# Optimization experiments

Hardware: AMD Instinct MI355X
Metric: run time of the kernel (lower is better)

## Reference

```python
import jax, jax.numpy as jnp
import numpy as np
from jax import lax
from jax.scipy.special import logsumexp

NUM_STATES = 32
INPUT_SIZE = 128
HIDDEN = 256
LN_EPS = 1e-5


def setup_inputs() -> dict:
    key = jax.random.key(0)
    ks = jax.random.split(key, 8)
    B, T = 32, 8192
    x = jax.random.normal(ks[0], (B, T, INPUT_SIZE), dtype=jnp.float32)
    # parameters (match torch defaults: initial_logits=zeros, transition_logits=2*I)
    initial_logits = jnp.zeros((NUM_STATES,), jnp.float32)
    transition_logits = 2.0 * jnp.eye(NUM_STATES, dtype=jnp.float32)
    W1 = jax.random.normal(ks[1], (INPUT_SIZE, HIDDEN), jnp.float32) / np.sqrt(INPUT_SIZE)
    b1 = jnp.zeros((HIDDEN,), jnp.float32)
    ln_g = jnp.ones((HIDDEN,), jnp.float32)
    ln_b = jnp.zeros((HIDDEN,), jnp.float32)
    W2 = jax.random.normal(ks[2], (HIDDEN, HIDDEN), jnp.float32) / np.sqrt(HIDDEN)
    b2 = jnp.zeros((HIDDEN,), jnp.float32)
    W3 = jax.random.normal(ks[3], (HIDDEN, NUM_STATES), jnp.float32) / np.sqrt(HIDDEN)
    b3 = jnp.zeros((NUM_STATES,), jnp.float32)
    return {"x": x, "initial_logits": initial_logits, "transition_logits": transition_logits,
            "W1": W1, "b1": b1, "ln_g": ln_g, "ln_b": ln_b, "W2": W2, "b2": b2, "W3": W3, "b3": b3}


def _emission_logprobs(x, W1, b1, ln_g, ln_b, W2, b2, W3, b3):
    h = x @ W1 + b1                                   # (B,T,H)
    mu = h.mean(-1, keepdims=True)
    var = ((h - mu) ** 2).mean(-1, keepdims=True)
    h = (h - mu) * lax.rsqrt(var + LN_EPS) * ln_g + ln_b
    h = jax.nn.gelu(h, approximate=False)             # torch nn.GELU default = exact
    h = jax.nn.gelu(h @ W2 + b2, approximate=False)
    logits = h @ W3 + b3                              # (B,T,S)  (dropout inactive at eval)
    return jax.nn.log_softmax(logits, axis=-1)


def reference(x, initial_logits, transition_logits, W1, b1, ln_g, ln_b, W2, b2, W3, b3):
    emissions = _emission_logprobs(x, W1, b1, ln_g, ln_b, W2, b2, W3, b3)  # (B,T,S)
    B = x.shape[0]
    trans = jax.nn.softmax(transition_logits, axis=-1)
    log_trans = jnp.log(trans + 1e-10)                               # (S,S)
    log_init = jnp.log(jax.nn.softmax(initial_logits) + 1e-10)       # (S,)

    alpha0 = log_init[None, :] + emissions[:, 0, :]                  # (B,S)
    em_rest = jnp.swapaxes(emissions[:, 1:, :], 0, 1)                # (T-1,B,S)

    # --- forward algorithm (log-sum-exp semiring scan over time) ---
    def fwd_step(alpha, em_t):
        a = em_t + logsumexp(alpha[:, :, None] + log_trans[None, :, :], axis=1)
        return a, a
    _, alphas_rest = lax.scan(fwd_step, alpha0, em_rest)             # (T-1,B,S)
    alphas = jnp.concatenate([alpha0[:, None, :], jnp.swapaxes(alphas_rest, 0, 1)], axis=1)  # (B,T,S)
    log_likelihood = logsumexp(alphas[:, -1, :], axis=-1)            # (B,)
    state_probs = jax.nn.softmax(alphas, axis=-1)

    # --- Viterbi (max-plus semiring scan + backtrace) ---
    def vit_step(vit, em_t):
        scores = vit[:, :, None] + log_trans[None, :, :]             # (B,S,S)
        return scores.max(axis=1) + em_t, scores.argmax(axis=1)
    vit_last, bps = lax.scan(vit_step, alpha0, em_rest)              # bps: (T-1,B,S) int32
    path_score = vit_last.max(axis=-1)
    last_state = vit_last.argmax(axis=-1)                            # (B,)
    bidx = jnp.arange(B)

    def bt_step(state, bp):
        prev = bp[bidx, state]
        return prev, prev
    _, path_prefix = lax.scan(bt_step, last_state, bps, reverse=True)  # (T-1,B)
    best_path = jnp.concatenate([jnp.swapaxes(path_prefix, 0, 1), last_state[:, None]], axis=1)  # (B,T)

    return (emissions, state_probs, log_likelihood, trans, best_path, path_score)
```

## Files before the change

### kernel.cpp

```cpp
#include <hip/hip_runtime.h>
#include <cstdint>
#include <cstddef>

#define TT 8192
#define SS 32

__device__ __forceinline__ float rsum32(float v){
    v += __shfl_xor(v,16); v += __shfl_xor(v,8); v += __shfl_xor(v,4);
    v += __shfl_xor(v,2);  v += __shfl_xor(v,1); return v;
}
__device__ __forceinline__ float rmax32(float v){
    v = fmaxf(v,__shfl_xor(v,16)); v = fmaxf(v,__shfl_xor(v,8)); v = fmaxf(v,__shfl_xor(v,4));
    v = fmaxf(v,__shfl_xor(v,2));  v = fmaxf(v,__shfl_xor(v,1)); return v;
}
__device__ __forceinline__ float rsum64(float v){
    v += __shfl_xor(v,32); v += __shfl_xor(v,16); v += __shfl_xor(v,8);
    v += __shfl_xor(v,4);  v += __shfl_xor(v,2);  v += __shfl_xor(v,1); return v;
}
__device__ __forceinline__ void lds_read32(const float* p, float* d){
    #pragma unroll
    for (int k=0;k<8;k++){
        float4 v = ((const float4*)p)[k];
        d[4*k+0]=v.x; d[4*k+1]=v.y; d[4*k+2]=v.z; d[4*k+3]=v.w;
    }
}
__device__ __forceinline__ float arr_sum32(const float* a){
    float s0=0.f,s1=0.f,s2=0.f,s3=0.f;
    #pragma unroll
    for (int k=0;k<32;k+=4){ s0+=a[k]; s1+=a[k+1]; s2+=a[k+2]; s3+=a[k+3]; }
    return (s0+s1)+(s2+s3);
}
__device__ __forceinline__ float arr_max32(const float* a){
    float s0=a[0],s1=a[1],s2=a[2],s3=a[3];
    #pragma unroll
    for (int k=4;k<32;k+=4){ s0=fmaxf(s0,a[k]); s1=fmaxf(s1,a[k+1]); s2=fmaxf(s2,a[k+2]); s3=fmaxf(s3,a[k+3]); }
    return fmaxf(fmaxf(s0,s1),fmaxf(s2,s3));
}
__device__ __forceinline__ float dot32(const float* a, const float* b){
    float s0=0.f,s1=0.f,s2=0.f,s3=0.f;
    #pragma unroll
    for (int k=0;k<32;k+=4){
        s0=fmaf(a[k],b[k],s0); s1=fmaf(a[k+1],b[k+1],s1);
        s2=fmaf(a[k+2],b[k+2],s2); s3=fmaf(a[k+3],b[k+3],s3);
    }
    return (s0+s1)+(s2+s3);
}
__device__ __forceinline__ float gelu_exact(float v){
    return 0.5f*v*(1.0f + erff(v*0.70710678118654752440f));
}

__global__ __launch_bounds__(1024) void hmm_prep(
    const float* __restrict__ il, const float* __restrict__ tl,
    float* __restrict__ trans, float* __restrict__ lt, float* __restrict__ li,
    float* __restrict__ LL, float* __restrict__ PS)
{
    const int tid = threadIdx.x;
    const int c = tid & 31;
    const float v = tl[tid];
    const float m = rmax32(v);
    const float e = expf(v - m);
    const float ssum = rsum32(e);
    const float t = e / ssum;
    trans[tid] = t;
    lt[tid] = logf(t + 1e-10f);
    if (tid < 32){
        const float iv = il[c];
        const float m2 = rmax32(iv);
        const float e2 = expf(iv - m2);
        const float s2 = rsum32(e2);
        li[c] = logf(e2/s2 + 1e-10f);
        LL[c] = 0.f;
        PS[c] = 0.f;
    }
}

__global__ __launch_bounds__(256, 5) void hmm_mlp(
    const float* __restrict__ x,
    const float* __restrict__ W1, const float* __restrict__ b1,
    const float* __restrict__ lng, const float* __restrict__ lnb,
    const float* __restrict__ W2, const float* __restrict__ b2,
    const float* __restrict__ W3, const float* __restrict__ b3,
    float* __restrict__ em_out)
{
    __shared__ float hbuf[8192];
    const int tid  = threadIdx.x;
    const int lane = tid & 63;
    const int wv   = tid >> 6;
    const int row0 = blockIdx.x << 5;
    const int r0   = wv << 3;
    const int c0   = lane << 2;

    const int r0u = __builtin_amdgcn_readfirstlane(r0);
    const float* xw = x + ((size_t)(row0 + r0u) << 7);

    float acc[8][4];
    #pragma unroll
    for (int i=0;i<8;i++){ acc[i][0]=0.f; acc[i][1]=0.f; acc[i][2]=0.f; acc[i][3]=0.f; }

    #pragma unroll 2
    for (int k4=0;k4<32;k4++){
        const float4 w0 = *(const float4*)&W1[((k4<<2)+0)*256 + c0];
        const float4 w1 = *(const float4*)&W1[((k4<<2)+1)*256 + c0];
        const float4 w2 = *(const float4*)&W1[((k4<<2)+2)*256 + c0];
        const float4 w3 = *(const float4*)&W1[((k4<<2)+3)*256 + c0];
        #pragma unroll
        for (int i=0;i<8;i++){
            const float4 xv = *(const float4*)(xw + (i<<7) + (k4<<2));
            acc[i][0]=fmaf(xv.x,w0.x,acc[i][0]); acc[i][1]=fmaf(xv.x,w0.y,acc[i][1]);
            acc[i][2]=fmaf(xv.x,w0.z,acc[i][2]); acc[i][3]=fmaf(xv.x,w0.w,acc[i][3]);
            acc[i][0]=fmaf(xv.y,w1.x,acc[i][0]); acc[i][1]=fmaf(xv.y,w1.y,acc[i][1]);
            acc[i][2]=fmaf(xv.y,w1.z,acc[i][2]); acc[i][3]=fmaf(xv.y,w1.w,acc[i][3]);
            acc[i][0]=fmaf(xv.z,w2.x,acc[i][0]); acc[i][1]=fmaf(xv.z,w2.y,acc[i][1]);
            acc[i][2]=fmaf(xv.z,w2.z,acc[i][2]); acc[i][3]=fmaf(xv.z,w2.w,acc[i][3]);
            acc[i][0]=fmaf(xv.w,w3.x,acc[i][0]); acc[i][1]=fmaf(xv.w,w3.y,acc[i][1]);
            acc[i][2]=fmaf(xv.w,w3.z,acc[i][2]); acc[i][3]=fmaf(xv.w,w3.w,acc[i][3]);
        }
    }

    {
        const float4 bb = *(const float4*)&b1[c0];
        const float4 gg = *(const float4*)&lng[c0];
        const float4 be = *(const float4*)&lnb[c0];
        #pragma unroll
        for (int i=0;i<8;i++){
            float a0=acc[i][0]+bb.x, a1=acc[i][1]+bb.y, a2=acc[i][2]+bb.z, a3=acc[i][3]+bb.w;
            float sm = (a0+a1)+(a2+a3);
            float sq = fmaf(a0,a0,fmaf(a1,a1,fmaf(a2,a2,a3*a3)));
            sm = rsum64(sm); sq = rsum64(sq);
            const float mu   = sm*(1.f/256.f);
            const float var  = sq*(1.f/256.f) - mu*mu;
            const float rstd = rsqrtf(var + 1e-5f);
            a0 = gelu_exact((a0-mu)*rstd*gg.x + be.x);
            a1 = gelu_exact((a1-mu)*rstd*gg.y + be.y);
            a2 = gelu_exact((a2-mu)*rstd*gg.z + be.z);
            a3 = gelu_exact((a3-mu)*rstd*gg.w + be.w);
            *(float4*)&hbuf[(r0+i)*256 + c0] = make_float4(a0,a1,a2,a3);
        }
    }

    #pragma unroll
    for (int i=0;i<8;i++){ acc[i][0]=0.f; acc[i][1]=0.f; acc[i][2]=0.f; acc[i][3]=0.f; }
    #pragma unroll 2
    for (int k4=0;k4<64;k4++){
        const float4 w0 = *(const float4*)&W2[((k4<<2)+0)*256 + c0];
        const float4 w1 = *(const float4*)&W2[((k4<<2)+1)*256 + c0];
        const float4 w2 = *(const float4*)&W2[((k4<<2)+2)*256 + c0];
        const float4 w3 = *(const float4*)&W2[((k4<<2)+3)*256 + c0];
        #pragma unroll
        for (int i=0;i<8;i++){
            const float4 hv = *(const float4*)&hbuf[(r0+i)*256 + (k4<<2)];
            acc[i][0]=fmaf(hv.x,w0.x,acc[i][0]); acc[i][1]=fmaf(hv.x,w0.y,acc[i][1]);
            acc[i][2]=fmaf(hv.x,w0.z,acc[i][2]); acc[i][3]=fmaf(hv.x,w0.w,acc[i][3]);
            acc[i][0]=fmaf(hv.y,w1.x,acc[i][0]); acc[i][1]=fmaf(hv.y,w1.y,acc[i][1]);
            acc[i][2]=fmaf(hv.y,w1.z,acc[i][2]); acc[i][3]=fmaf(hv.y,w1.w,acc[i][3]);
            acc[i][0]=fmaf(hv.z,w2.x,acc[i][0]); acc[i][1]=fmaf(hv.z,w2.y,acc[i][1]);
            acc[i][2]=fmaf(hv.z,w2.z,acc[i][2]); acc[i][3]=fmaf(hv.z,w2.w,acc[i][3]);
            acc[i][0]=fmaf(hv.w,w3.x,acc[i][0]); acc[i][1]=fmaf(hv.w,w3.y,acc[i][1]);
            acc[i][2]=fmaf(hv.w,w3.z,acc[i][2]); acc[i][3]=fmaf(hv.w,w3.w,acc[i][3]);
        }
    }
    {
        const float4 bv = *(const float4*)&b2[c0];
        #pragma unroll
        for (int i=0;i<8;i++){
            const int r = r0+i;
            const float a0 = gelu_exact(acc[i][0]+bv.x);
            const float a1 = gelu_exact(acc[i][1]+bv.y);
            const float a2 = gelu_exact(acc[i][2]+bv.z);
            const float a3 = gelu_exact(acc[i][3]+bv.w);
            *(float4*)&hbuf[r*256 + (c0 ^ ((r&7)<<2))] = make_float4(a0,a1,a2,a3);
        }
    }

    {
        const int r3  = tid >> 3;
        const int cg  = tid & 7;
        const int sw3 = (r3 & 7) << 2;
        float a3[4] = {0.f,0.f,0.f,0.f};
        const float4* W34 = (const float4*)W3;
        #pragma unroll 2
        for (int k4=0;k4<64;k4++){
            const float4 hv = *(const float4*)&hbuf[r3*256 + ((k4<<2) ^ sw3)];
            const float h[4] = {hv.x,hv.y,hv.z,hv.w};
            #pragma unroll
            for (int kk=0;kk<4;kk++){
                const float4 w = W34[((k4<<2)+kk)*8 + cg];
                a3[0]=fmaf(h[kk],w.x,a3[0]); a3[1]=fmaf(h[kk],w.y,a3[1]);
                a3[2]=fmaf(h[kk],w.z,a3[2]); a3[3]=fmaf(h[kk],w.w,a3[3]);
            }
        }
        const float4 b3v = ((const float4*)b3)[cg];
        a3[0]+=b3v.x; a3[1]+=b3v.y; a3[2]+=b3v.z; a3[3]+=b3v.w;
        float m = fmaxf(fmaxf(a3[0],a3[1]),fmaxf(a3[2],a3[3]));
        m = fmaxf(m,__shfl_xor(m,4)); m = fmaxf(m,__shfl_xor(m,2)); m = fmaxf(m,__shfl_xor(m,1));
        float se = expf(a3[0]-m)+expf(a3[1]-m)+expf(a3[2]-m)+expf(a3[3]-m);
        se += __shfl_xor(se,4); se += __shfl_xor(se,2); se += __shfl_xor(se,1);
        const float lz = m + logf(se);
        float4 o = make_float4(a3[0]-lz, a3[1]-lz, a3[2]-lz, a3[3]-lz);
        *(float4*)&em_out[((size_t)(row0+r3))*32 + (cg<<2)] = o;
    }
}

__global__ __launch_bounds__(256) void hmm_fwd(
    const float* __restrict__ em, const float* __restrict__ trans,
    const float* __restrict__ li, float* __restrict__ sp, float* __restrict__ LL)
{
    __shared__ float Ab[8][32];
    const int lane = threadIdx.x & 63;
    const int s = lane & 31;
    const int ci = ((threadIdx.x >> 6) << 1) | (lane >> 5);
    const int cid = (blockIdx.x << 3) + ci;
    const int b = cid >> 7;
    const int c = cid & 127;
    const int t0 = c << 6;

    float tc[32];
    #pragma unroll
    for (int k=0;k<32;k++) tc[k] = trans[(k<<5) + s];
    float* A = Ab[ci];
    const float* emb = em + (size_t)b*(TT*SS);
    const float li_s = li[s];

    A[s] = 0.03125f;
    asm volatile("s_waitcnt lgkmcnt(0)" ::: "memory");
    __builtin_amdgcn_wave_barrier();

    float sig = 0.f;
    float araw_prev = 0.f;

    const int tws = t0 - 64;
    float pe[8];
    #pragma unroll
    for (int j=0;j<8;j++){ int tt = tws + j; tt = tt < 0 ? 0 : tt; pe[j] = emb[(tt<<5) + s]; }

    #pragma unroll 1
    for (int g=0; g<8; g++){
        float ce[8];
        #pragma unroll
        for (int j=0;j<8;j++) ce[j] = pe[j];
        #pragma unroll
        for (int j=0;j<8;j++){ int tt = tws + ((g+1)<<3) + j; tt = tt < 0 ? 0 : tt; pe[j] = emb[(tt<<5) + s]; }
        #pragma unroll
        for (int j=0;j<8;j++){
            float Av[32];
            lds_read32(A, Av);
            const float sum = arr_sum32(Av);
            const float val = dot32(Av, tc);
            const float rs = 1.0f / sum;
            const float e = __expf(ce[j]);
            const float araw = val * rs * e;
            __builtin_amdgcn_wave_barrier();
            A[s] = araw;
            asm volatile("s_waitcnt lgkmcnt(0)" ::: "memory");
            __builtin_amdgcn_wave_barrier();
        }
    }

    #pragma unroll 1
    for (int g=0; g<8; g++){
        float ce[8];
        #pragma unroll
        for (int j=0;j<8;j++) ce[j] = pe[j];
        #pragma unroll
        for (int j=0;j<8;j++){ int tt = t0 + ((g+1)<<3) + j; tt = tt > (TT-1) ? (TT-1) : tt; pe[j] = emb[(tt<<5) + s]; }
        #pragma unroll
        for (int j=0;j<8;j++){
            const int i = (g<<3) + j;
            const int t = t0 + i;
            float Av[32];
            lds_read32(A, Av);
            const float sum = arr_sum32(Av);
            const float val = dot32(Av, tc);
            const float rs = 1.0f / sum;
            if (i > 0){
                sp[((size_t)b*TT + (t-1))*SS + s] = araw_prev * rs;
                sig += __logf(sum);
            }
            const float e = __expf(ce[j]);
            float araw = val * rs * e;
            if (c == 0 && i == 0) araw = __expf(li_s) * e;
            __builtin_amdgcn_wave_barrier();
            A[s] = araw;
            asm volatile("s_waitcnt lgkmcnt(0)" ::: "memory");
            __builtin_amdgcn_wave_barrier();
            araw_prev = araw;
        }
    }
    {
        float Av[32];
        lds_read32(A, Av);
        const float sum = arr_sum32(Av);
        const float rs = 1.0f / sum;
        sp[((size_t)b*TT + (t0+63))*SS + s] = araw_prev * rs;
        sig += __logf(sum);
    }
    if (s == 0) atomicAdd(&LL[b], sig);
}

__global__ __launch_bounds__(256) void hmm_vit(
    const float* __restrict__ em, const float* __restrict__ lt,
    const float* __restrict__ li, unsigned char* __restrict__ bps,
    float* __restrict__ PS, int* __restrict__ last_state)
{
    __shared__ float Vb[8][32];
    const int lane = threadIdx.x & 63;
    const int s = lane & 31;
    const int ci = ((threadIdx.x >> 6) << 1) | (lane >> 5);
    const int cid = (blockIdx.x << 3) + ci;
    const int b = cid >> 7;
    const int c = cid & 127;
    const int t0 = c << 6;

    float ltc[32];
    #pragma unroll
    for (int k=0;k<32;k++) ltc[k] = lt[(k<<5) + s];
    float* V = Vb[ci];
    const float* emb = em + (size_t)b*(TT*SS);
    const float li_s = li[s];

    V[s] = 0.f;
    asm volatile("s_waitcnt lgkmcnt(0)" ::: "memory");
    __builtin_amdgcn_wave_barrier();

    float delta = 0.f;

    const int tws = t0 - 128;
    float pe[8];
    #pragma unroll
    for (int j=0;j<8;j++){ int tt = tws + j; tt = tt < 0 ? 0 : tt; pe[j] = emb[(tt<<5) + s]; }

    #pragma unroll 1
    for (int g=0; g<16; g++){
        float ce[8];
        #pragma unroll
        for (int j=0;j<8;j++) ce[j] = pe[j];
        #pragma unroll
        for (int j=0;j<8;j++){ int tt = tws + ((g+1)<<3) + j; tt = tt < 0 ? 0 : tt; pe[j] = emb[(tt<<5) + s]; }
        #pragma unroll
        for (int j=0;j<8;j++){
            float Vv[32];
            lds_read32(V, Vv);
            float b0=-3.0e38f,b1v=-3.0e38f,b2v=-3.0e38f,b3v=-3.0e38f;
            #pragma unroll
            for (int k=0;k<32;k+=4){
                b0  = fmaxf(b0,  Vv[k]+ltc[k]);
                b1v = fmaxf(b1v, Vv[k+1]+ltc[k+1]);
                b2v = fmaxf(b2v, Vv[k+2]+ltc[k+2]);
                b3v = fmaxf(b3v, Vv[k+3]+ltc[k+3]);
            }
            float v = fmaxf(fmaxf(b0,b1v),fmaxf(b2v,b3v)) + ce[j];
            if (j == 7) v -= arr_max32(Vv);
            __builtin_amdgcn_wave_barrier();
            V[s] = v;
            asm volatile("s_waitcnt lgkmcnt(0)" ::: "memory");
            __builtin_amdgcn_wave_barrier();
        }
    }
    {
        float Vv[32];
        lds_read32(V, Vv);
        const float mm = arr_max32(Vv);
        __builtin_amdgcn_wave_barrier();
        V[s] = Vv[s] - mm;
        asm volatile("s_waitcnt lgkmcnt(0)" ::: "memory");
        __builtin_amdgcn_wave_barrier();
    }

    #pragma unroll 1
    for (int g=0; g<8; g++){
        float ce[8];
        #pragma unroll
        for (int j=0;j<8;j++) ce[j] = pe[j];
        #pragma unroll
        for (int j=0;j<8;j++){ int tt = t0 + ((g+1)<<3) + j; tt = tt > (TT-1) ? (TT-1) : tt; pe[j] = emb[(tt<<5) + s]; }
        #pragma unroll
        for (int j=0;j<8;j++){
            const int i = (g<<3) + j;
            const int t = t0 + i;
            float Vv[32];
            lds_read32(V, Vv);
            float B0=Vv[0]+ltc[0], B1=Vv[1]+ltc[1], B2=Vv[2]+ltc[2], B3=Vv[3]+ltc[3];
            int I0=0,I1=1,I2=2,I3=3;
            #pragma unroll
            for (int k=4;k<32;k+=4){
                float q0=Vv[k]+ltc[k];     if (q0>B0){B0=q0;I0=k;}
                float q1=Vv[k+1]+ltc[k+1]; if (q1>B1){B1=q1;I1=k+1;}
                float q2=Vv[k+2]+ltc[k+2]; if (q2>B2){B2=q2;I2=k+2;}
                float q3=Vv[k+3]+ltc[k+3]; if (q3>B3){B3=q3;I3=k+3;}
            }
            float best = B0; int bi = I0;
            if (B1>best || (B1==best && I1<bi)){best=B1;bi=I1;}
            if (B2>best || (B2==best && I2<bi)){best=B2;bi=I2;}
            if (B3>best || (B3==best && I3<bi)){best=B3;bi=I3;}
            float mmc = 0.f;
            if (j == 0){ mmc = arr_max32(Vv); delta += mmc; }
            float v;
            if (c == 0 && i == 0){
                v = li_s + ce[j];
            } else {
                v = best + ce[j] - mmc;
                bps[((size_t)b*TT + t)*SS + s] = (unsigned char)bi;
            }
            __builtin_amdgcn_wave_barrier();
            V[s] = v;
            asm volatile("s_waitcnt lgkmcnt(0)" ::: "memory");
            __builtin_amdgcn_wave_barrier();
        }
    }
    {
        float Vv[32];
        lds_read32(V, Vv);
        const float mm = arr_max32(Vv);
        delta += mm;
        if (c == 127){
            float best = Vv[0]; int bi = 0;
            #pragma unroll
            for (int k=1;k<32;k++){ if (Vv[k] > best){ best = Vv[k]; bi = k; } }
            if (s == 0) last_state[b] = bi;
        }
        if (s == 0) atomicAdd(&PS[b], delta);
    }
}

__global__ __launch_bounds__(64) void hmm_btc(
    const unsigned char* __restrict__ bps, unsigned char* __restrict__ pos,
    unsigned char* __restrict__ gmap)
{
    __shared__ unsigned char bp[8192];
    const int b = blockIdx.x >> 5;
    const int cb = blockIdx.x & 31;
    const int tbase = cb << 8;
    {
        const uint4* src = (const uint4*)(bps + ((size_t)b*TT + tbase)*SS);
        uint4* dst = (uint4*)bp;
        #pragma unroll
        for (int l=0;l<8;l++) dst[threadIdx.x + (l<<6)] = src[threadIdx.x + (l<<6)];
    }
    __syncthreads();
    if (threadIdx.x < 32){
        int cur = threadIdx.x;
        unsigned char* pc = pos + (((size_t)b<<5) + cb)*8192;
        #pragma unroll 1
        for (int t=255; t>=0; t--){
            pc[(t<<5) + threadIdx.x] = (unsigned char)cur;
            if ((tbase + t) >= 1) cur = bp[(t<<5) + cur];
        }
        gmap[(((b<<5) + cb)<<5) + threadIdx.x] = (unsigned char)cur;
    }
}

__global__ __launch_bounds__(256) void hmm_btb(
    const unsigned char* __restrict__ gmap, const int* __restrict__ last_state,
    unsigned char* __restrict__ e_tab)
{
    __shared__ unsigned char gl[32768];
    #pragma unroll
    for (int l=0;l<8;l++) ((uint4*)gl)[threadIdx.x + (l<<8)] = ((const uint4*)gmap)[threadIdx.x + (l<<8)];
    __syncthreads();
    if (threadIdx.x < 32){
        const int b = threadIdx.x;
        int s = last_state[b];
        #pragma unroll 1
        for (int cb=31; cb>=1; cb--){
            e_tab[(b<<5)+cb] = (unsigned char)s;
            s = gl[(((b<<5)+cb)<<5) + s];
        }
        e_tab[b<<5] = (unsigned char)s;
    }
}

__global__ __launch_bounds__(256) void hmm_btf(
    const unsigned char* __restrict__ pos, const unsigned char* __restrict__ e_tab,
    float* __restrict__ path)
{
    const int i = blockIdx.x*256 + threadIdx.x;
    const int b = i >> 13;
    const int t = i & (TT-1);
    const int cb = t >> 8;
    const int e = e_tab[(b<<5) + cb];
    const unsigned char v = pos[((((size_t)b<<5) + cb)<<13) + ((t & 255)<<5) + e];
    path[i] = (float)v;
}

extern "C" void kernel_launch(void* const* d_in, const int* in_sizes, int n_in,
                              void* d_out, int out_size, void* d_ws, size_t ws_size,
                              hipStream_t stream)
{
    const float* x   = (const float*)d_in[0];
    const float* il  = (const float*)d_in[1];
    const float* tl  = (const float*)d_in[2];
    const float* W1  = (const float*)d_in[3];
    const float* b1  = (const float*)d_in[4];
    const float* lng = (const float*)d_in[5];
    const float* lnb = (const float*)d_in[6];
    const float* W2  = (const float*)d_in[7];
    const float* b2  = (const float*)d_in[8];
    const float* W3  = (const float*)d_in[9];
    const float* b3  = (const float*)d_in[10];

    float* out   = (float*)d_out;
    float* em    = out;
    float* sp    = out + 8388608;
    float* LL    = out + 16777216;
    float* trans = out + 16777248;
    float* path  = out + 16778272;
    float* PS    = out + 17040416;

    char* wsb = (char*)d_ws;
    float* lt            = (float*)(wsb);
    float* li            = (float*)(wsb + 4096);
    int* last_state      = (int*)(wsb + 4224);
    unsigned char* e_tab = (unsigned char*)(wsb + 4352);
    unsigned char* bps   = (unsigned char*)(wsb + 8192);
    unsigned char* pos   = (unsigned char*)(wsb + 8192 + 8388608);
    unsigned char* gmap  = (unsigned char*)(wsb + 8192 + 16777216);

    hmm_prep<<<1, 1024, 0, stream>>>(il, tl, trans, lt, li, LL, PS);
    hmm_mlp<<<8192, 256, 0, stream>>>(x, W1, b1, lng, lnb, W2, b2, W3, b3, em);
    hmm_fwd<<<512, 256, 0, stream>>>(em, trans, li, sp, LL);
    hmm_vit<<<512, 256, 0, stream>>>(em, lt, li, bps, PS, last_state);
    hmm_btc<<<1024, 64, 0, stream>>>(bps, pos, gmap);
    hmm_btb<<<1, 256, 0, stream>>>(gmap, last_state, e_tab);
    hmm_btf<<<1024, 256, 0, stream>>>(pos, e_tab, path);
}
```

Measured before the change: 1.432 ms.

## Give each MLP wave 16 rows with wave-private swizzled LDS and per-wave output layer

The MLP kernel drops from 256-thread blocks of four waves with 8 rows each to 128-thread blocks of two waves with 16 rows each. Each wave works on its own swizzled slice of LDS, so every W1/W2 weight load is reused across twice as many rows. The final 256x32 layer becomes a per-wave split-K over two half-warps combined with a shuffle, which removes the cross-wave LDS dependency. In exchange each thread holds 64 accumulators, which raises register pressure and lowers occupancy, and half the lanes sit idle during the output stores.

```diff
diff --git a/kernel.cpp b/kernel.cpp
--- a/kernel.cpp
+++ b/kernel.cpp
@@ -74,7 +74,7 @@
     }
 }
 
-__global__ __launch_bounds__(256, 5) void hmm_mlp(
+__global__ __launch_bounds__(128, 4) void hmm_mlp(
     const float* __restrict__ x,
     const float* __restrict__ W1, const float* __restrict__ b1,
     const float* __restrict__ lng, const float* __restrict__ lnb,
@@ -86,16 +86,15 @@
     const int tid  = threadIdx.x;
     const int lane = tid & 63;
     const int wv   = tid >> 6;
-    const int row0 = blockIdx.x << 5;
-    const int r0   = wv << 3;
-    const int c0   = lane << 2;
-
-    const int r0u = __builtin_amdgcn_readfirstlane(r0);
-    const float* xw = x + ((size_t)(row0 + r0u) << 7);
-
-    float acc[8][4];
-    #pragma unroll
-    for (int i=0;i<8;i++){ acc[i][0]=0.f; acc[i][1]=0.f; acc[i][2]=0.f; acc[i][3]=0.f; }
+    const int rowbase = (blockIdx.x << 5) + (wv << 4);
+    float* hb = hbuf + (wv << 12);
+    const int c0 = lane << 2;
+
+    const float* xw = x + ((size_t)__builtin_amdgcn_readfirstlane(rowbase) << 7);
+
+    float acc[16][4];
+    #pragma unroll
+    for (int i=0;i<16;i++){ acc[i][0]=0.f; acc[i][1]=0.f; acc[i][2]=0.f; acc[i][3]=0.f; }
 
     #pragma unroll 2
     for (int k4=0;k4<32;k4++){
@@ -104,7 +103,7 @@
         const float4 w2 = *(const float4*)&W1[((k4<<2)+2)*256 + c0];
         const float4 w3 = *(const float4*)&W1[((k4<<2)+3)*256 + c0];
         #pragma unroll
-        for (int i=0;i<8;i++){
+        for (int i=0;i<16;i++){
             const float4 xv = *(const float4*)(xw + (i<<7) + (k4<<2));
             acc[i][0]=fmaf(xv.x,w0.x,acc[i][0]); acc[i][1]=fmaf(xv.x,w0.y,acc[i][1]);
             acc[i][2]=fmaf(xv.x,w0.z,acc[i][2]); acc[i][3]=fmaf(xv.x,w0.w,acc[i][3]);
@@ -122,7 +121,7 @@
         const float4 gg = *(const float4*)&lng[c0];
         const float4 be = *(const float4*)&lnb[c0];
         #pragma unroll
-        for (int i=0;i<8;i++){
+        for (int i=0;i<16;i++){
             float a0=acc[i][0]+bb.x, a1=acc[i][1]+bb.y, a2=acc[i][2]+bb.z, a3=acc[i][3]+bb.w;
             float sm = (a0+a1)+(a2+a3);
             float sq = fmaf(a0,a0,fmaf(a1,a1,fmaf(a2,a2,a3*a3)));
@@ -134,12 +133,12 @@
             a1 = gelu_exact((a1-mu)*rstd*gg.y + be.y);
             a2 = gelu_exact((a2-mu)*rstd*gg.z + be.z);
             a3 = gelu_exact((a3-mu)*rstd*gg.w + be.w);
-            *(float4*)&hbuf[(r0+i)*256 + c0] = make_float4(a0,a1,a2,a3);
-        }
-    }
-
-    #pragma unroll
-    for (int i=0;i<8;i++){ acc[i][0]=0.f; acc[i][1]=0.f; acc[i][2]=0.f; acc[i][3]=0.f; }
+            *(float4*)&hb[(i<<8) + (c0 ^ ((i&7)<<2))] = make_float4(a0,a1,a2,a3);
+        }
+    }
+
+    #pragma unroll
+    for (int i=0;i<16;i++){ acc[i][0]=0.f; acc[i][1]=0.f; acc[i][2]=0.f; acc[i][3]=0.f; }
     #pragma unroll 2
     for (int k4=0;k4<64;k4++){
         const float4 w0 = *(const float4*)&W2[((k4<<2)+0)*256 + c0];
@@ -147,8 +146,8 @@
         const float4 w2 = *(const float4*)&W2[((k4<<2)+2)*256 + c0];
         const float4 w3 = *(const float4*)&W2[((k4<<2)+3)*256 + c0];
         #pragma unroll
-        for (int i=0;i<8;i++){
-            const float4 hv = *(const float4*)&hbuf[(r0+i)*256 + (k4<<2)];
+        for (int i=0;i<16;i++){
+            const float4 hv = *(const float4*)&hb[(i<<8) + (((k4<<2)) ^ ((i&7)<<2))];
             acc[i][0]=fmaf(hv.x,w0.x,acc[i][0]); acc[i][1]=fmaf(hv.x,w0.y,acc[i][1]);
             acc[i][2]=fmaf(hv.x,w0.z,acc[i][2]); acc[i][3]=fmaf(hv.x,w0.w,acc[i][3]);
             acc[i][0]=fmaf(hv.y,w1.x,acc[i][0]); acc[i][1]=fmaf(hv.y,w1.y,acc[i][1]);
@@ -162,42 +161,46 @@
     {
         const float4 bv = *(const float4*)&b2[c0];
         #pragma unroll
-        for (int i=0;i<8;i++){
-            const int r = r0+i;
+        for (int i=0;i<16;i++){
             const float a0 = gelu_exact(acc[i][0]+bv.x);
             const float a1 = gelu_exact(acc[i][1]+bv.y);
             const float a2 = gelu_exact(acc[i][2]+bv.z);
             const float a3 = gelu_exact(acc[i][3]+bv.w);
-            *(float4*)&hbuf[r*256 + (c0 ^ ((r&7)<<2))] = make_float4(a0,a1,a2,a3);
-        }
-    }
-
-    {
-        const int r3  = tid >> 3;
-        const int cg  = tid & 7;
-        const int sw3 = (r3 & 7) << 2;
-        float a3[4] = {0.f,0.f,0.f,0.f};
-        const float4* W34 = (const float4*)W3;
+            *(float4*)&hb[(i<<8) + (c0 ^ ((i&7)<<2))] = make_float4(a0,a1,a2,a3);
+        }
+    }
+
+    {
+        const int cS = lane & 31;
+        const int kh = lane >> 5;
+        float lg[16];
+        #pragma unroll
+        for (int i=0;i<16;i++) lg[i] = 0.f;
         #pragma unroll 2
-        for (int k4=0;k4<64;k4++){
-            const float4 hv = *(const float4*)&hbuf[r3*256 + ((k4<<2) ^ sw3)];
-            const float h[4] = {hv.x,hv.y,hv.z,hv.w};
+        for (int k4=0;k4<32;k4++){
+            const int kb = (kh<<7) + (k4<<2);
+            const int slot = (kb>>2);
+            const float wv0 = W3[(kb+0)*32 + cS];
+            const float wv1 = W3[(kb+1)*32 + cS];
+            const float wv2 = W3[(kb+2)*32 + cS];
+            const float wv3 = W3[(kb+3)*32 + cS];
             #pragma unroll
-            for (int kk=0;kk<4;kk++){
-                const float4 w = W34[((k4<<2)+kk)*8 + cg];
-                a3[0]=fmaf(h[kk],w.x,a3[0]); a3[1]=fmaf(h[kk],w.y,a3[1]);
-                a3[2]=fmaf(h[kk],w.z,a3[2]); a3[3]=fmaf(h[kk],w.w,a3[3]);
+            for (int i=0;i<16;i++){
+                const float4 hv = *(const float4*)&hb[(i<<8) + ((slot<<2) ^ ((i&7)<<2))];
+                lg[i]=fmaf(hv.x,wv0,lg[i]); lg[i]=fmaf(hv.y,wv1,lg[i]);
+                lg[i]=fmaf(hv.z,wv2,lg[i]); lg[i]=fmaf(hv.w,wv3,lg[i]);
             }
         }
-        const float4 b3v = ((const float4*)b3)[cg];
-        a3[0]+=b3v.x; a3[1]+=b3v.y; a3[2]+=b3v.z; a3[3]+=b3v.w;
-        float m = fmaxf(fmaxf(a3[0],a3[1]),fmaxf(a3[2],a3[3]));
-        m = fmaxf(m,__shfl_xor(m,4)); m = fmaxf(m,__shfl_xor(m,2)); m = fmaxf(m,__shfl_xor(m,1));
-        float se = expf(a3[0]-m)+expf(a3[1]-m)+expf(a3[2]-m)+expf(a3[3]-m);
-        se += __shfl_xor(se,4); se += __shfl_xor(se,2); se += __shfl_xor(se,1);
-        const float lz = m + logf(se);
-        float4 o = make_float4(a3[0]-lz, a3[1]-lz, a3[2]-lz, a3[3]-lz);
-        *(float4*)&em_out[((size_t)(row0+r3))*32 + (cg<<2)] = o;
+        const float b3v = b3[cS];
+        #pragma unroll
+        for (int i=0;i<16;i++){
+            float v = lg[i] + __shfl_xor(lg[i], 32) + b3v;
+            const float m = rmax32(v);
+            const float e = expf(v - m);
+            const float se = rsum32(e);
+            const float o = v - (m + logf(se));
+            if (lane < 32) em_out[((size_t)(rowbase + i) << 5) + cS] = o;
+        }
     }
 }
 
@@ -516,7 +519,7 @@
     unsigned char* gmap  = (unsigned char*)(wsb + 8192 + 16777216);
 
     hmm_prep<<<1, 1024, 0, stream>>>(il, tl, trans, lt, li, LL, PS);
-    hmm_mlp<<<8192, 256, 0, stream>>>(x, W1, b1, lng, lnb, W2, b2, W3, b3, em);
+    hmm_mlp<<<8192, 128, 0, stream>>>(x, W1, b1, lng, lnb, W2, b2, W3, b3, em);
     hmm_fwd<<<512, 256, 0, stream>>>(em, trans, li, sp, LL);
     hmm_vit<<<512, 256, 0, stream>>>(em, lt, li, bps, PS, last_state);
     hmm_btc<<<1024, 64, 0, stream>>>(bps, pos, gmap);
```

Measured after the change: 1.232 ms. 14.0% less time.
